# Performance work log

Measured on AMD Instinct MI355X. Metric: run time of the kernel, lower is better.

The kernel has to match this reference:

```python
import math
import jax, jax.numpy as jnp
import numpy as np

BATCH, LENGTH, D_MODEL, D_STATE = 8, 2048, 1024, 64
DT_MIN, DT_MAX = 1e-3, 1e-1


def setup_inputs() -> dict:
    key = jax.random.key(0)
    k1, k2, k3, k4 = jax.random.split(key, 4)
    x = jax.random.normal(k1, (BATCH, LENGTH, D_MODEL), dtype=jnp.float32)
    # dt_init == 'random': log_dt ~ U[log(dt_min), log(dt_max)], dt_scale = 1.0
    log_dt = jax.random.uniform(k2, (D_MODEL,), dtype=jnp.float32) * (
        math.log(DT_MAX) - math.log(DT_MIN)) + math.log(DT_MIN)
    scale = 1.0 / math.sqrt(D_STATE)
    B = jax.random.normal(k3, (D_MODEL, D_STATE), dtype=jnp.float32) * scale
    C = jax.random.normal(k4, (D_MODEL, D_STATE), dtype=jnp.float32) * scale
    D = jnp.ones((D_MODEL,), dtype=jnp.float32)
    return {"x": x, "log_dt": log_dt, "B": B, "C": C, "D": D}


def reference(x, log_dt, B, C, D):
    """S4DKernel.forward(x, mode='conv') -> y of shape [batch, length, d_model]."""
    d_model, d_state = B.shape
    length = x.shape[1]
    # A buffer: -0.5 * [1..d_state]
    A = -0.5 * jnp.arange(1, d_state + 1, dtype=jnp.float32)  # [N]
    # ZOH discretization
    dt = jnp.exp(log_dt)                       # [D]
    dtA = dt[:, None] * A[None, :]             # [D, N]
    A_bar = jnp.exp(dtA)                       # [D, N]
    B_bar = jnp.expm1(dtA) / A[None, :] * B    # [D, N]
    # Vandermonde kernel: K[d, k] = sum_n C[d,n] * B_bar[d,n] * A_bar[d,n]^k
    k_range = jnp.arange(length, dtype=jnp.float32)                 # [L]
    log_A_bar = jnp.log(jnp.clip(A_bar, 1e-10))                     # [D, N]
    powers = jnp.exp(log_A_bar[:, :, None] * k_range[None, None, :])  # [D, N, L]
    kernel = jnp.einsum('dn,dnk->dk', C * B_bar, powers)            # [D, L]
    # FFT convolution (linear conv via 2L-point FFT)
    x_t = jnp.swapaxes(x, 1, 2)                # [B, D, L]
    fft_size = 2 * length
    x_f = jnp.fft.rfft(x_t, n=fft_size)        # [B, D, L+1]
    k_f = jnp.fft.rfft(kernel, n=fft_size)     # [D, L+1]
    y = jnp.fft.irfft(x_f * k_f[None], n=fft_size)[..., :length]
    y = y + D[None, :, None] * x_t             # skip connection
    return jnp.swapaxes(y, 1, 2)               # [B, L, D]
```

## Files before the change

### kernel.cpp

```cpp
#include <hip/hip_runtime.h>
#include <math.h>


namespace {
constexpr int kBatch = 8;
constexpr int kLen   = 2048;
constexpr int kD     = 1024;
constexpr int kN     = 64;

template <int T>
struct Cfg {
  static constexpr int  kC     = kLen / T;
  static constexpr long kU     = (long)kBatch * kC * kN * kD;
  static constexpr long kAOff  = kU;
  static constexpr long kCbOff = kAOff + (long)kN * kD;
  static constexpr long kAtOff = kCbOff + (long)kN * kD;
  static constexpr long kBytes = (kAtOff + (long)kN * kD) * 4;
};
}

template <int T>
__global__ void s4d_coef_kernel(const float* __restrict__ log_dt,
                                const float* __restrict__ Bm,
                                const float* __restrict__ Cm,
                                float* __restrict__ ws) {
  int tid = blockIdx.x * blockDim.x + threadIdx.x;
  int d = tid & (kD - 1);
  int n = tid >> 10;
  float dt  = expf(log_dt[d]);
  float An  = -0.5f * (float)(n + 1);
  float dtA = dt * An;
  float a   = expf(dtA);
  float bbar = (expm1f(dtA) / An) * Bm[d * kN + n];
  float cb   = Cm[d * kN + n] * bbar;
  float aT   = expf(dtA * (float)T);
  ws[Cfg<T>::kAOff  + (long)n * kD + d] = a;
  ws[Cfg<T>::kCbOff + (long)n * kD + d] = cb;
  ws[Cfg<T>::kAtOff + (long)n * kD + d] = aT;
}

template <int T>
__global__ __launch_bounds__(256, T == 32 ? 8 : 4) void s4d_state_kernel(
    const float* __restrict__ x, float* __restrict__ ws) {
  constexpr int C = Cfg<T>::kC;
  int tid = blockIdx.x * blockDim.x + threadIdx.x;
  int d  = tid & (kD - 1);
  int bc = tid >> 10;
  int b  = bc / C;
  int c  = bc % C;

  const float* xp = x + ((long)b * kLen + (long)c * T) * kD + d;
  float xv[T];
#pragma unroll
  for (int t = 0; t < T; ++t) xv[t] = xp[(long)t * kD];

  const float* ap = ws + Cfg<T>::kAOff + d;
  float* up = ws + ((long)(b * C + c) * kN) * kD + d;
#pragma unroll 4
  for (int n = 0; n < kN; ++n) {
    float a = ap[(long)n * kD];
    float h = 0.f;
#pragma unroll
    for (int t = 0; t < T; ++t) h = fmaf(h, a, xv[t]);
    up[(long)n * kD] = h;
  }
}

template <int T>
__global__ void s4d_scan_kernel(float* __restrict__ ws) {
  constexpr int C = Cfg<T>::kC;
  int tid = blockIdx.x * blockDim.x + threadIdx.x;
  int d  = tid & (kD - 1);
  int bn = tid >> 10;
  int n  = bn & (kN - 1);
  int b  = bn >> 6;
  float aT = ws[Cfg<T>::kAtOff + (long)n * kD + d];
  float* up = ws + ((long)b * C * kN + n) * kD + d;
  const long cstride = (long)kN * kD;
  float s = 0.f;
#pragma unroll 1
  for (int c = 0; c < C; ++c) {
    float u = up[(long)c * cstride];
    up[(long)c * cstride] = s;
    s = fmaf(aT, s, u);
  }
}

template <int T>
__global__ __launch_bounds__(256, T == 32 ? 5 : 2) void s4d_out_kernel(
    const float* __restrict__ x, const float* __restrict__ Dv,
    float* __restrict__ y, const float* __restrict__ ws) {
  constexpr int C = Cfg<T>::kC;
  int tid = blockIdx.x * blockDim.x + threadIdx.x;
  int d  = tid & (kD - 1);
  int bc = tid >> 10;
  int b  = bc / C;
  int c  = bc % C;

  const float* xp = x + ((long)b * kLen + (long)c * T) * kD + d;
  float xv[T];
#pragma unroll
  for (int t = 0; t < T; ++t) xv[t] = xp[(long)t * kD];

  float Dd = Dv[d];
  float acc[T];
#pragma unroll
  for (int t = 0; t < T; ++t) acc[t] = Dd * xv[t];

  const float* ap  = ws + Cfg<T>::kAOff + d;
  const float* cbp = ws + Cfg<T>::kCbOff + d;
  const float* sp  = ws + ((long)(b * C + c) * kN) * kD + d;

  float an = ap[0], cbn = cbp[0], hn = sp[0];
#pragma unroll 2
  for (int n = 0; n < kN; ++n) {
    float a2  = ap[(long)(n + 1) * kD];
    float cb2 = cbp[(long)(n + 1) * kD];
    float s2  = sp[(long)(n + 1) * kD];
    float a = an, cb = cbn, h = hn;
#pragma unroll
    for (int t = 0; t < T; ++t) {
      h = fmaf(h, a, xv[t]);
      acc[t] = fmaf(cb, h, acc[t]);
    }
    an = a2; cbn = cb2; hn = s2;
  }

  float* yp = y + ((long)b * kLen + (long)c * T) * kD + d;
#pragma unroll
  for (int t = 0; t < T; ++t) yp[(long)t * kD] = acc[t];
}

template <int T>
static void launch_all(const float* x, const float* log_dt, const float* Bm,
                       const float* Cm, const float* Dv, float* y, float* ws,
                       hipStream_t stream) {
  constexpr int C = Cfg<T>::kC;
  hipLaunchKernelGGL((s4d_coef_kernel<T>), dim3((kN * kD) / 256), dim3(256), 0,
                     stream, log_dt, Bm, Cm, ws);
  hipLaunchKernelGGL((s4d_state_kernel<T>), dim3((kBatch * C * kD) / 256),
                     dim3(256), 0, stream, x, ws);
  hipLaunchKernelGGL((s4d_scan_kernel<T>), dim3((kBatch * kN * kD) / 256),
                     dim3(256), 0, stream, ws);
  hipLaunchKernelGGL((s4d_out_kernel<T>), dim3((kBatch * C * kD) / 256),
                     dim3(256), 0, stream, x, Dv, y, ws);
}

extern "C" void kernel_launch(void* const* d_in, const int* in_sizes, int n_in,
                              void* d_out, int out_size, void* d_ws,
                              size_t ws_size, hipStream_t stream) {
  const float* x      = (const float*)d_in[0];
  const float* log_dt = (const float*)d_in[1];
  const float* Bm     = (const float*)d_in[2];
  const float* Cm     = (const float*)d_in[3];
  const float* Dv     = (const float*)d_in[4];
  float* y  = (float*)d_out;
  float* ws = (float*)d_ws;

  if (ws_size >= (size_t)Cfg<32>::kBytes) {
    launch_all<32>(x, log_dt, Bm, Cm, Dv, y, ws, stream);
  } else {
    launch_all<64>(x, log_dt, Bm, Cm, Dv, y, ws, stream);
  }
}
```

Before: 251.6 us.

## Interleave state recurrences across groups of modes to expose ILP

The state and output kernels now process groups of 16 and 8 state modes together, interleaving their independent recurrences inside the time loop. Previously each mode ran as one serial FMA chain. The per-thread array of x values is gone: x is reloaded from global memory (mostly cache) once per mode group. This breaks the serial dependency chain and frees registers, and the output kernel's occupancy hint rises from 5 to 6. The cost is repeated x loads per group and a longer dependent chain on each acc[t] within a group.

```diff
diff --git a/kernel.cpp b/kernel.cpp
--- a/kernel.cpp
+++ b/kernel.cpp
@@ -42,7 +42,8 @@
 template <int T>
 __global__ __launch_bounds__(256, T == 32 ? 8 : 4) void s4d_state_kernel(
     const float* __restrict__ x, float* __restrict__ ws) {
-  constexpr int C = Cfg<T>::kC;
+  constexpr int C  = Cfg<T>::kC;
+  constexpr int NG = 16;
   int tid = blockIdx.x * blockDim.x + threadIdx.x;
   int d  = tid & (kD - 1);
   int bc = tid >> 10;
@@ -50,24 +51,30 @@
   int c  = bc % C;
 
   const float* xp = x + ((long)b * kLen + (long)c * T) * kD + d;
-  float xv[T];
-#pragma unroll
-  for (int t = 0; t < T; ++t) xv[t] = xp[(long)t * kD];
-
   const float* ap = ws + Cfg<T>::kAOff + d;
   float* up = ws + ((long)(b * C + c) * kN) * kD + d;
-#pragma unroll 4
-  for (int n = 0; n < kN; ++n) {
-    float a = ap[(long)n * kD];
-    float h = 0.f;
+
+#pragma unroll 1
+  for (int g = 0; g < kN; g += NG) {
+    float a[NG], h[NG];
 #pragma unroll
-    for (int t = 0; t < T; ++t) h = fmaf(h, a, xv[t]);
-    up[(long)n * kD] = h;
+    for (int i = 0; i < NG; ++i) {
+      a[i] = ap[(long)(g + i) * kD];
+      h[i] = 0.f;
+    }
+#pragma unroll
+    for (int t = 0; t < T; ++t) {
+      float xt = xp[(long)t * kD];
+#pragma unroll
+      for (int i = 0; i < NG; ++i) h[i] = fmaf(h[i], a[i], xt);
+    }
+#pragma unroll
+    for (int i = 0; i < NG; ++i) up[(long)(g + i) * kD] = h[i];
   }
 }
 
 template <int T>
-__global__ void s4d_scan_kernel(float* __restrict__ ws) {
+__global__ __launch_bounds__(256) void s4d_scan_kernel(float* __restrict__ ws) {
   constexpr int C = Cfg<T>::kC;
   int tid = blockIdx.x * blockDim.x + threadIdx.x;
   int d  = tid & (kD - 1);
@@ -87,10 +94,11 @@
 }
 
 template <int T>
-__global__ __launch_bounds__(256, T == 32 ? 5 : 2) void s4d_out_kernel(
+__global__ __launch_bounds__(256, T == 32 ? 6 : 2) void s4d_out_kernel(
     const float* __restrict__ x, const float* __restrict__ Dv,
     float* __restrict__ y, const float* __restrict__ ws) {
-  constexpr int C = Cfg<T>::kC;
+  constexpr int C  = Cfg<T>::kC;
+  constexpr int NG = 8;
   int tid = blockIdx.x * blockDim.x + threadIdx.x;
   int d  = tid & (kD - 1);
   int bc = tid >> 10;
@@ -98,32 +106,35 @@
   int c  = bc % C;
 
   const float* xp = x + ((long)b * kLen + (long)c * T) * kD + d;
-  float xv[T];
-#pragma unroll
-  for (int t = 0; t < T; ++t) xv[t] = xp[(long)t * kD];
+  float Dd = Dv[d];
 
-  float Dd = Dv[d];
   float acc[T];
 #pragma unroll
-  for (int t = 0; t < T; ++t) acc[t] = Dd * xv[t];
+  for (int t = 0; t < T; ++t) acc[t] = Dd * xp[(long)t * kD];
 
   const float* ap  = ws + Cfg<T>::kAOff + d;
   const float* cbp = ws + Cfg<T>::kCbOff + d;
   const float* sp  = ws + ((long)(b * C + c) * kN) * kD + d;
 
-  float an = ap[0], cbn = cbp[0], hn = sp[0];
-#pragma unroll 2
-  for (int n = 0; n < kN; ++n) {
-    float a2  = ap[(long)(n + 1) * kD];
-    float cb2 = cbp[(long)(n + 1) * kD];
-    float s2  = sp[(long)(n + 1) * kD];
-    float a = an, cb = cbn, h = hn;
+#pragma unroll 1
+  for (int g = 0; g < kN; g += NG) {
+    float a[NG], cb[NG], h[NG];
+#pragma unroll
+    for (int i = 0; i < NG; ++i) {
+      long o = (long)(g + i) * kD;
+      a[i]  = ap[o];
+      cb[i] = cbp[o];
+      h[i]  = sp[o];
+    }
 #pragma unroll
     for (int t = 0; t < T; ++t) {
-      h = fmaf(h, a, xv[t]);
-      acc[t] = fmaf(cb, h, acc[t]);
+      float xt = xp[(long)t * kD];
+#pragma unroll
+      for (int i = 0; i < NG; ++i) {
+        h[i]   = fmaf(h[i], a[i], xt);
+        acc[t] = fmaf(cb[i], h[i], acc[t]);
+      }
     }
-    an = a2; cbn = cb2; hn = s2;
   }
 
   float* yp = y + ((long)b * kLen + (long)c * T) * kD + d;
```

After: 552.2 us. 119% more time.
